# Kernel optimization log

Measured on AMD Instinct MI355X. Metric: run time of the kernel, lower is better.

The kernel has to match this reference:

```python
import jax, jax.numpy as jnp
import numpy as np

B, N, T, D = 4, 1000, 12, 64
HID, EF = 128, 64
E = 64000
STEP = 0.1

def setup_inputs() -> dict:
    key = jax.random.key(0)
    ks = jax.random.split(key, 16)
    s = 0.05
    return {
        'x': jax.random.normal(ks[0], (B, N, T, D), dtype=jnp.float32),
        'batch_idx': jax.random.randint(ks[1], (E,), 0, B, dtype=jnp.int32),
        'sender_idx': jax.random.randint(ks[2], (E,), 0, N, dtype=jnp.int32),
        'receiver_idx': jax.random.randint(ks[3], (E,), 0, N, dtype=jnp.int32),
        'A1_w': jax.random.normal(ks[4], (D, HID), dtype=jnp.float32) * s,
        'A1_b': jax.random.normal(ks[5], (HID,), dtype=jnp.float32) * s,
        'A2_w': jax.random.normal(ks[6], (D, HID), dtype=jnp.float32) * s,
        'A2_b': jax.random.normal(ks[7], (HID,), dtype=jnp.float32) * s,
        'A3_w': jax.random.normal(ks[8], (HID, EF), dtype=jnp.float32) * s,
        'A3_b': jax.random.normal(ks[9], (EF,), dtype=jnp.float32) * s,
        'A4_w': jax.random.normal(ks[10], (EF, D), dtype=jnp.float32) * s,
        'A4_b': jax.random.normal(ks[11], (D,), dtype=jnp.float32) * s,
    }

def reference(x, batch_idx, sender_idx, receiver_idx,
              A1_w, A1_b, A2_w, A2_b, A3_w, A3_b, A4_w, A4_b):
    # x: [B, N, T, D]; edge list gathers (equivalent to adj.nonzero)
    x_sender = x[batch_idx, sender_idx]      # [E, T, D]
    x_receiver = x[batch_idx, receiver_idx]  # [E, T, D]

    def edge_mlp(a, b):
        # A3(relu(A1(a) + A2(b))), applied per edge-time element
        h = jax.nn.relu(a @ A1_w + A1_b + b @ A2_w + A2_b)
        return h @ A3_w + A3_b

    z_ij = edge_mlp(x_sender, x_receiver)
    z_ji = edge_mlp(x_receiver, x_sender)
    v_ij_pre = jax.nn.relu(z_ij - z_ji) @ A4_w + A4_b  # [E, T, D]

    seg_send = batch_idx * N + sender_idx  # [E]
    # numerically-stable segment softmax over outgoing edges of each sender
    max_logits = jax.ops.segment_max(v_ij_pre, seg_send, num_segments=B * N)
    exp_centered = jnp.exp(v_ij_pre - max_logits[seg_send])
    denom = jax.ops.segment_sum(exp_centered, seg_send, num_segments=B * N)
    v_ij = exp_centered / (denom[seg_send] + 1e-12)  # [E, T, D]

    messages = v_ij * x_sender
    seg_recv = batch_idx * N + receiver_idx
    inbound = jax.ops.segment_sum(messages, seg_recv, num_segments=B * N)
    inbound = inbound.reshape(B, N, T, D)

    x_updated = x + STEP * (inbound - x)
    return x_updated, v_ij
```

## Files before the change

kernel.cpp:

```cpp
#include <hip/hip_runtime.h>
#include <math.h>

#define BB 4
#define NN 1000
#define TT 12
#define DD 64
#define HIDN 128
#define EFN 64
#define EE 64000
#define BN (BB*NN)
#define ROWS (BN*TT)
#define TD (TT*DD)
#define STEPF 0.1f
#define MAXSEG 32

typedef __attribute__((ext_vector_type(8))) short bfrag8;
typedef __attribute__((ext_vector_type(8))) unsigned short u16x8;
typedef __attribute__((ext_vector_type(4))) float f32x4;

__device__ __forceinline__ float bf2f(unsigned short u) {
    union { unsigned int i; float f; } p; p.i = ((unsigned int)u) << 16; return p.f;
}
__device__ __forceinline__ unsigned short f2bf(float x) {
    union { float f; unsigned int i; } p; p.f = x;
    unsigned int r = (p.i + 0x7FFFu + ((p.i >> 16) & 1u)) >> 16;
    return (unsigned short)r;
}

__global__ __launch_bounds__(256) void k_zero(int* __restrict__ p, int n) {
    int i = blockIdx.x * 256 + threadIdx.x;
    if (i < n) p[i] = 0;
}

__global__ __launch_bounds__(256) void k_count(const int* __restrict__ bi,
                                               const int* __restrict__ si,
                                               const int* __restrict__ ri,
                                               int* __restrict__ cnt_s,
                                               int* __restrict__ cnt_r) {
    int e = blockIdx.x * 256 + threadIdx.x;
    if (e < EE) {
        int b = bi[e];
        atomicAdd(&cnt_s[b * NN + si[e]], 1);
        atomicAdd(&cnt_r[b * NN + ri[e]], 1);
    }
}

__global__ __launch_bounds__(256) void k_scan(const int* __restrict__ cnt_s,
                                              const int* __restrict__ cnt_r,
                                              int* __restrict__ rp_s, int* __restrict__ rp_r,
                                              int* __restrict__ cur_s, int* __restrict__ cur_r) {
    const int* cnt = blockIdx.x ? cnt_r : cnt_s;
    int* rp  = blockIdx.x ? rp_r  : rp_s;
    int* cur = blockIdx.x ? cur_r : cur_s;
    __shared__ int part[256];
    int tid = threadIdx.x;
    const int chunk = 16;
    int bgn = tid * chunk;
    int end = min(bgn + chunk, BN);
    int s = 0;
    for (int i = bgn; i < end; ++i) s += cnt[i];
    part[tid] = s;
    __syncthreads();
    for (int off = 1; off < 256; off <<= 1) {
        int v = part[tid];
        if (tid >= off) v += part[tid - off];
        __syncthreads();
        part[tid] = v;
        __syncthreads();
    }
    int run = tid ? part[tid - 1] : 0;
    for (int i = bgn; i < end; ++i) { rp[i] = run; cur[i] = run; run += cnt[i]; }
    if (tid == 255) rp[BN] = part[255];
}

__global__ __launch_bounds__(256) void k_fill(const int* __restrict__ bi,
                                              const int* __restrict__ si,
                                              const int* __restrict__ ri,
                                              int* __restrict__ cur_s, int* __restrict__ cur_r,
                                              int* __restrict__ el_s, int* __restrict__ el_r) {
    int e = blockIdx.x * 256 + threadIdx.x;
    if (e < EE) {
        int b = bi[e];
        int ps = atomicAdd(&cur_s[b * NN + si[e]], 1);
        el_s[ps] = e;
        int pr = atomicAdd(&cur_r[b * NN + ri[e]], 1);
        el_r[pr] = e;
    }
}

__global__ __launch_bounds__(256) void k_prep_w(const float* __restrict__ A3_w,
                                                const float* __restrict__ A4_w,
                                                unsigned short* __restrict__ W3f,
                                                unsigned short* __restrict__ W4f) {
    int i = blockIdx.x * 256 + threadIdx.x;
    if (i < 8192) {
        int j = i & 7, lane = (i >> 3) & 63, nt = (i >> 9) & 3, kt = i >> 11;
        int k = kt * 32 + (lane >> 4) * 8 + j;
        int n = nt * 16 + (lane & 15);
        W3f[i] = f2bf(A3_w[k * 64 + n]);
    } else if (i < 12288) {
        int ii = i - 8192;
        int j = ii & 7, lane = (ii >> 3) & 63, nt = (ii >> 9) & 3, kt = ii >> 11;
        int k = kt * 32 + (lane >> 4) * 8 + j;
        int n = nt * 16 + (lane & 15);
        W4f[ii] = f2bf(A4_w[k * 64 + n]);
    }
}

__global__ __launch_bounds__(256) void k_node_proj(const float* __restrict__ x,
                                                   const float* __restrict__ A1_w,
                                                   const float* __restrict__ A1_b,
                                                   const float* __restrict__ A2_w,
                                                   const float* __restrict__ A2_b,
                                                   unsigned short* __restrict__ Q1,
                                                   unsigned short* __restrict__ Q2) {
    __shared__ float xs[16][64];
    int tid = threadIdx.x;
    int row0 = blockIdx.x * 16;
    {
        int i = tid * 4;
        int r = i >> 6, k = i & 63;
        *(float4*)&xs[r][k] = *(const float4*)&x[(size_t)(row0 + r) * 64 + k];
    }
    __syncthreads();
    int h = tid & 127;
    int w = tid >> 7;
    const float* W = w ? A2_w : A1_w;
    float bias = w ? A2_b[h] : A1_b[h];
    float acc[16];
#pragma unroll
    for (int r = 0; r < 16; ++r) acc[r] = 0.f;
    for (int k = 0; k < 64; ++k) {
        float wv = W[k * 128 + h];
#pragma unroll
        for (int r = 0; r < 16; ++r) acc[r] += xs[r][k] * wv;
    }
    unsigned short* Qo = w ? Q2 : Q1;
    for (int r = 0; r < 16; ++r) Qo[(size_t)(row0 + r) * 128 + h] = f2bf(acc[r] + bias);
}

__global__ __launch_bounds__(256) void k_edge_seg(const unsigned short* __restrict__ Q1,
                                                  const unsigned short* __restrict__ Q2,
                                                  const int* __restrict__ bi,
                                                  const int* __restrict__ si,
                                                  const int* __restrict__ ri,
                                                  const int* __restrict__ rp_s,
                                                  const int* __restrict__ el_s,
                                                  const unsigned short* __restrict__ W3f,
                                                  const unsigned short* __restrict__ W4f,
                                                  const float* __restrict__ A4_b,
                                                  float* __restrict__ v) {
    __shared__ unsigned short Vseg[MAXSEG][12][68];
    __shared__ __align__(16) float Hs[4][16][68];

    int seg = blockIdx.x;
    int beg = rp_s[seg], end = rp_s[seg + 1];
    int S = end - beg;
    if (S == 0) return;

    int tid  = threadIdx.x;
    int lane = tid & 63;
    int wv   = tid >> 6;
    int quad = lane >> 4;
    int m    = lane & 15;
    int kbase = quad * 8;

    bfrag8 w3[4][4], w4[2][4];
#pragma unroll
    for (int kt = 0; kt < 4; ++kt)
#pragma unroll
        for (int nt = 0; nt < 4; ++nt)
            w3[kt][nt] = *(const bfrag8*)&W3f[((kt * 4 + nt) * 64 + lane) * 8];
#pragma unroll
    for (int kt = 0; kt < 2; ++kt)
#pragma unroll
        for (int nt = 0; nt < 4; ++nt)
            w4[kt][nt] = *(const bfrag8*)&W4f[((kt * 4 + nt) * 64 + lane) * 8];
    float b4[4];
#pragma unroll
    for (int nt = 0; nt < 4; ++nt) b4[nt] = A4_b[nt * 16 + m];

    const bfrag8 zfrag = {0, 0, 0, 0, 0, 0, 0, 0};

    for (int li = wv; li < S; li += 4) {
        int e = el_s[beg + li];
        int b = bi[e];
        int sn = b * NN + si[e];
        int rn = b * NN + ri[e];

        bfrag8 af[4];
        if (m < 12) {
            const unsigned short* p1s = Q1 + (size_t)sn * (TT * HIDN) + m * 128 + kbase;
            const unsigned short* p2r = Q2 + (size_t)rn * (TT * HIDN) + m * 128 + kbase;
            const unsigned short* p1r = Q1 + (size_t)rn * (TT * HIDN) + m * 128 + kbase;
            const unsigned short* p2s = Q2 + (size_t)sn * (TT * HIDN) + m * 128 + kbase;
#pragma unroll
            for (int kt = 0; kt < 4; ++kt) {
                u16x8 x1 = *(const u16x8*)(p1s + kt * 32);
                u16x8 x2 = *(const u16x8*)(p2r + kt * 32);
                u16x8 x3 = *(const u16x8*)(p1r + kt * 32);
                u16x8 x4 = *(const u16x8*)(p2s + kt * 32);
                union { bfrag8 v; unsigned short u[8]; } fr;
#pragma unroll
                for (int j = 0; j < 8; ++j) {
                    float a = bf2f(x1[j]) + bf2f(x2[j]);
                    float c = bf2f(x3[j]) + bf2f(x4[j]);
                    fr.u[j] = f2bf(fmaxf(a, 0.f) - fmaxf(c, 0.f));
                }
                af[kt] = fr.v;
            }
        } else {
#pragma unroll
            for (int kt = 0; kt < 4; ++kt) af[kt] = zfrag;
        }

        f32x4 acc[4];
#pragma unroll
        for (int nt = 0; nt < 4; ++nt) acc[nt] = (f32x4){0.f, 0.f, 0.f, 0.f};
#pragma unroll
        for (int kt = 0; kt < 4; ++kt)
#pragma unroll
            for (int nt = 0; nt < 4; ++nt)
                acc[nt] = __builtin_amdgcn_mfma_f32_16x16x32_bf16(af[kt], w3[kt][nt], acc[nt], 0, 0, 0);

#pragma unroll
        for (int nt = 0; nt < 4; ++nt)
#pragma unroll
            for (int r = 0; r < 4; ++r)
                Hs[wv][quad * 4 + r][nt * 16 + m] = fmaxf(acc[nt][r], 0.f);

        bfrag8 hf[2];
#pragma unroll
        for (int kt = 0; kt < 2; ++kt) {
            const float* hp = &Hs[wv][m][kt * 32 + kbase];
            float4 h0 = *(const float4*)hp;
            float4 h1 = *(const float4*)(hp + 4);
            union { bfrag8 v; unsigned short u[8]; } fr;
            fr.u[0] = f2bf(h0.x); fr.u[1] = f2bf(h0.y);
            fr.u[2] = f2bf(h0.z); fr.u[3] = f2bf(h0.w);
            fr.u[4] = f2bf(h1.x); fr.u[5] = f2bf(h1.y);
            fr.u[6] = f2bf(h1.z); fr.u[7] = f2bf(h1.w);
            hf[kt] = fr.v;
        }

#pragma unroll
        for (int nt = 0; nt < 4; ++nt) {
            f32x4 o = (f32x4){b4[nt], b4[nt], b4[nt], b4[nt]};
#pragma unroll
            for (int kt = 0; kt < 2; ++kt)
                o = __builtin_amdgcn_mfma_f32_16x16x32_bf16(hf[kt], w4[kt][nt], o, 0, 0, 0);
            if (quad < 3) {
                if (li < MAXSEG) {
#pragma unroll
                    for (int r = 0; r < 4; ++r)
                        Vseg[li][quad * 4 + r][nt * 16 + m] = f2bf(o[r]);
                } else {
                    size_t ebase = (size_t)e * TD;
#pragma unroll
                    for (int r = 0; r < 4; ++r)
                        v[ebase + (quad * 4 + r) * 64 + nt * 16 + m] = o[r];
                }
            }
        }
    }
    __syncthreads();

    int d  = tid & 63;
    int tb = tid >> 6;
    int nL = min(S, MAXSEG);

    float mj[3] = {-1e30f, -1e30f, -1e30f};
    for (int i = 0; i < nL; ++i) {
#pragma unroll
        for (int jj = 0; jj < 3; ++jj)
            mj[jj] = fmaxf(mj[jj], bf2f(Vseg[i][tb + 4 * jj][d]));
    }
    for (int i = MAXSEG; i < S; ++i) {
        size_t ebase = (size_t)el_s[beg + i] * TD;
#pragma unroll
        for (int jj = 0; jj < 3; ++jj)
            mj[jj] = fmaxf(mj[jj], v[ebase + (tb + 4 * jj) * 64 + d]);
    }

    float sj[3] = {0.f, 0.f, 0.f};
    for (int i = 0; i < nL; ++i) {
#pragma unroll
        for (int jj = 0; jj < 3; ++jj)
            sj[jj] += __expf(bf2f(Vseg[i][tb + 4 * jj][d]) - mj[jj]);
    }
    for (int i = MAXSEG; i < S; ++i) {
        size_t ebase = (size_t)el_s[beg + i] * TD;
#pragma unroll
        for (int jj = 0; jj < 3; ++jj)
            sj[jj] += __expf(v[ebase + (tb + 4 * jj) * 64 + d] - mj[jj]);
    }

    float inv[3];
#pragma unroll
    for (int jj = 0; jj < 3; ++jj) inv[jj] = 1.f / (sj[jj] + 1e-12f);

    for (int i = 0; i < nL; ++i) {
        size_t ebase = (size_t)el_s[beg + i] * TD;
#pragma unroll
        for (int jj = 0; jj < 3; ++jj)
            v[ebase + (tb + 4 * jj) * 64 + d] =
                __expf(bf2f(Vseg[i][tb + 4 * jj][d]) - mj[jj]) * inv[jj];
    }
    for (int i = MAXSEG; i < S; ++i) {
        size_t ebase = (size_t)el_s[beg + i] * TD;
#pragma unroll
        for (int jj = 0; jj < 3; ++jj) {
            size_t a = ebase + (tb + 4 * jj) * 64 + d;
            v[a] = __expf(v[a] - mj[jj]) * inv[jj];
        }
    }
}

__global__ __launch_bounds__(256) void k_aggregate(const int* __restrict__ rp_r,
                                                   const int* __restrict__ el_r,
                                                   const int* __restrict__ si,
                                                   const float* __restrict__ x,
                                                   const float* __restrict__ v,
                                                   float* __restrict__ xout) {
    int node = blockIdx.x;
    int beg = rp_r[node], end = rp_r[node + 1];
    int tid = threadIdx.x;
    int b = node / NN;
    __shared__ int e_l[256];
    __shared__ int sb_l[256];
    float acc[3] = {0.f, 0.f, 0.f};
    for (int c = beg; c < end; c += 256) {
        int cnt = min(end - c, 256);
        if (tid < cnt) {
            int e = el_r[c + tid];
            e_l[tid] = e;
            sb_l[tid] = (b * NN + si[e]) * TD;
        }
        __syncthreads();
        for (int i = 0; i < cnt; ++i) {
            size_t vb = (size_t)e_l[i] * TD;
            int sb = sb_l[i];
#pragma unroll
            for (int jj = 0; jj < 3; ++jj) {
                int j = tid + jj * 256;
                acc[jj] += v[vb + j] * x[sb + j];
            }
        }
        __syncthreads();
    }
    size_t nb = (size_t)node * TD;
#pragma unroll
    for (int jj = 0; jj < 3; ++jj) {
        int j = tid + jj * 256;
        float xv = x[nb + j];
        xout[nb + j] = xv + STEPF * (acc[jj] - xv);
    }
}

extern "C" void kernel_launch(void* const* d_in, const int* in_sizes, int n_in,
                              void* d_out, int out_size, void* d_ws, size_t ws_size,
                              hipStream_t stream) {
    const float* x    = (const float*)d_in[0];
    const int*   bi   = (const int*)d_in[1];
    const int*   si   = (const int*)d_in[2];
    const int*   ri   = (const int*)d_in[3];
    const float* A1_w = (const float*)d_in[4];
    const float* A1_b = (const float*)d_in[5];
    const float* A2_w = (const float*)d_in[6];
    const float* A2_b = (const float*)d_in[7];
    const float* A3_w = (const float*)d_in[8];
    const float* A4_w = (const float*)d_in[10];
    const float* A4_b = (const float*)d_in[11];

    float* xout = (float*)d_out;
    float* v    = (float*)d_out + (size_t)BN * TD;

    unsigned short* Q1  = (unsigned short*)d_ws;
    unsigned short* Q2  = Q1 + (size_t)ROWS * HIDN;
    unsigned short* W3f = Q2 + (size_t)ROWS * HIDN;
    unsigned short* W4f = W3f + 8192;
    int* cnt_s = (int*)(W4f + 4096);
    int* cnt_r = cnt_s + BN;
    int* rp_s  = cnt_r + BN;
    int* rp_r  = rp_s + BN + 1;
    int* cur_s = rp_r + BN + 1;
    int* cur_r = cur_s + BN;
    int* el_s  = cur_r + BN;
    int* el_r  = el_s + EE;

    k_zero<<<(2 * BN + 255) / 256, 256, 0, stream>>>(cnt_s, 2 * BN);
    k_count<<<EE / 256, 256, 0, stream>>>(bi, si, ri, cnt_s, cnt_r);
    k_scan<<<2, 256, 0, stream>>>(cnt_s, cnt_r, rp_s, rp_r, cur_s, cur_r);
    k_fill<<<EE / 256, 256, 0, stream>>>(bi, si, ri, cur_s, cur_r, el_s, el_r);
    k_prep_w<<<48, 256, 0, stream>>>(A3_w, A4_w, W3f, W4f);
    k_node_proj<<<ROWS / 16, 256, 0, stream>>>(x, A1_w, A1_b, A2_w, A2_b, Q1, Q2);
    k_edge_seg<<<BN, 256, 0, stream>>>(Q1, Q2, bi, si, ri, rp_s, el_s, W3f, W4f, A4_b, v);
    k_aggregate<<<BN, 256, 0, stream>>>(rp_r, el_r, si, x, v, xout);
}
```

Before: 494.9 us.

## Switch edge MLP to fp16 packed math, hoist sender rows, shrink LDS for occupancy

Intermediates Q1/Q2, weights and the staged logits move from bf16 to fp16, so the pre-activation combine runs as packed half-precision vector adds and max instead of per-element float conversions, and the MFMAs use the f16 variant. The sender row pointers are hoisted out of the edge loop because every edge in a segment shares the same sender and batch, which removes the bi/si gathers. The hidden staging buffer becomes fp16 and MAXSEG drops to 27, shrinking LDS so launch_bounds(256,3) can fit three blocks per CU. The cost is fp16 range and precision on the intermediates, and segments longer than 27 edges spill more often to global memory.

```diff
diff --git a/kernel.cpp b/kernel.cpp
--- a/kernel.cpp
+++ b/kernel.cpp
@@ -12,19 +12,17 @@
 #define ROWS (BN*TT)
 #define TD (TT*DD)
 #define STEPF 0.1f
-#define MAXSEG 32
-
-typedef __attribute__((ext_vector_type(8))) short bfrag8;
-typedef __attribute__((ext_vector_type(8))) unsigned short u16x8;
-typedef __attribute__((ext_vector_type(4))) float f32x4;
-
-__device__ __forceinline__ float bf2f(unsigned short u) {
-    union { unsigned int i; float f; } p; p.i = ((unsigned int)u) << 16; return p.f;
-}
-__device__ __forceinline__ unsigned short f2bf(float x) {
-    union { float f; unsigned int i; } p; p.f = x;
-    unsigned int r = (p.i + 0x7FFFu + ((p.i >> 16) & 1u)) >> 16;
-    return (unsigned short)r;
+#define MAXSEG 27
+
+typedef _Float16 f16x8 __attribute__((ext_vector_type(8)));
+typedef float f32x4 __attribute__((ext_vector_type(4)));
+
+__device__ __forceinline__ unsigned short f2h(float x) {
+    _Float16 h = (_Float16)x;
+    return __builtin_bit_cast(unsigned short, h);
+}
+__device__ __forceinline__ float h2f(unsigned short u) {
+    return (float)__builtin_bit_cast(_Float16, u);
 }
 
 __global__ __launch_bounds__(256) void k_zero(int* __restrict__ p, int n) {
@@ -97,13 +95,13 @@
         int j = i & 7, lane = (i >> 3) & 63, nt = (i >> 9) & 3, kt = i >> 11;
         int k = kt * 32 + (lane >> 4) * 8 + j;
         int n = nt * 16 + (lane & 15);
-        W3f[i] = f2bf(A3_w[k * 64 + n]);
+        W3f[i] = f2h(A3_w[k * 64 + n]);
     } else if (i < 12288) {
         int ii = i - 8192;
         int j = ii & 7, lane = (ii >> 3) & 63, nt = (ii >> 9) & 3, kt = ii >> 11;
         int k = kt * 32 + (lane >> 4) * 8 + j;
         int n = nt * 16 + (lane & 15);
-        W4f[ii] = f2bf(A4_w[k * 64 + n]);
+        W4f[ii] = f2h(A4_w[k * 64 + n]);
     }
 }
 
@@ -136,22 +134,20 @@
         for (int r = 0; r < 16; ++r) acc[r] += xs[r][k] * wv;
     }
     unsigned short* Qo = w ? Q2 : Q1;
-    for (int r = 0; r < 16; ++r) Qo[(size_t)(row0 + r) * 128 + h] = f2bf(acc[r] + bias);
-}
-
-__global__ __launch_bounds__(256) void k_edge_seg(const unsigned short* __restrict__ Q1,
-                                                  const unsigned short* __restrict__ Q2,
-                                                  const int* __restrict__ bi,
-                                                  const int* __restrict__ si,
-                                                  const int* __restrict__ ri,
-                                                  const int* __restrict__ rp_s,
-                                                  const int* __restrict__ el_s,
-                                                  const unsigned short* __restrict__ W3f,
-                                                  const unsigned short* __restrict__ W4f,
-                                                  const float* __restrict__ A4_b,
-                                                  float* __restrict__ v) {
+    for (int r = 0; r < 16; ++r) Qo[(size_t)(row0 + r) * 128 + h] = f2h(acc[r] + bias);
+}
+
+__global__ __launch_bounds__(256, 3) void k_edge_seg(const unsigned short* __restrict__ Q1,
+                                                     const unsigned short* __restrict__ Q2,
+                                                     const int* __restrict__ ri,
+                                                     const int* __restrict__ rp_s,
+                                                     const int* __restrict__ el_s,
+                                                     const unsigned short* __restrict__ W3f,
+                                                     const unsigned short* __restrict__ W4f,
+                                                     const float* __restrict__ A4_b,
+                                                     float* __restrict__ v) {
     __shared__ unsigned short Vseg[MAXSEG][12][68];
-    __shared__ __align__(16) float Hs[4][16][68];
+    __shared__ __align__(16) _Float16 Hs[4][16][72];
 
     int seg = blockIdx.x;
     int beg = rp_s[seg], end = rp_s[seg + 1];
@@ -164,54 +160,54 @@
     int quad = lane >> 4;
     int m    = lane & 15;
     int kbase = quad * 8;
-
-    bfrag8 w3[4][4], w4[2][4];
+    int b    = seg / NN;
+
+    f16x8 w3[4][4], w4[2][4];
 #pragma unroll
     for (int kt = 0; kt < 4; ++kt)
 #pragma unroll
         for (int nt = 0; nt < 4; ++nt)
-            w3[kt][nt] = *(const bfrag8*)&W3f[((kt * 4 + nt) * 64 + lane) * 8];
+            w3[kt][nt] = *(const f16x8*)&W3f[((kt * 4 + nt) * 64 + lane) * 8];
 #pragma unroll
     for (int kt = 0; kt < 2; ++kt)
 #pragma unroll
         for (int nt = 0; nt < 4; ++nt)
-            w4[kt][nt] = *(const bfrag8*)&W4f[((kt * 4 + nt) * 64 + lane) * 8];
+            w4[kt][nt] = *(const f16x8*)&W4f[((kt * 4 + nt) * 64 + lane) * 8];
     float b4[4];
 #pragma unroll
     for (int nt = 0; nt < 4; ++nt) b4[nt] = A4_b[nt * 16 + m];
 
-    const bfrag8 zfrag = {0, 0, 0, 0, 0, 0, 0, 0};
+    const f16x8 hz = {0, 0, 0, 0, 0, 0, 0, 0};
+
+    const unsigned short* ps1 = Q1 + (size_t)seg * (TT * HIDN) + m * 128 + kbase;
+    const unsigned short* ps2 = Q2 + (size_t)seg * (TT * HIDN) + m * 128 + kbase;
 
     for (int li = wv; li < S; li += 4) {
         int e = el_s[beg + li];
-        int b = bi[e];
-        int sn = b * NN + si[e];
         int rn = b * NN + ri[e];
 
-        bfrag8 af[4];
+        f16x8 g[4];
         if (m < 12) {
-            const unsigned short* p1s = Q1 + (size_t)sn * (TT * HIDN) + m * 128 + kbase;
-            const unsigned short* p2r = Q2 + (size_t)rn * (TT * HIDN) + m * 128 + kbase;
-            const unsigned short* p1r = Q1 + (size_t)rn * (TT * HIDN) + m * 128 + kbase;
-            const unsigned short* p2s = Q2 + (size_t)sn * (TT * HIDN) + m * 128 + kbase;
+            const unsigned short* pr1 = Q1 + (size_t)rn * (TT * HIDN) + m * 128 + kbase;
+            const unsigned short* pr2 = Q2 + (size_t)rn * (TT * HIDN) + m * 128 + kbase;
+            f16x8 s1[4], s2[4], r1[4], r2[4];
 #pragma unroll
             for (int kt = 0; kt < 4; ++kt) {
-                u16x8 x1 = *(const u16x8*)(p1s + kt * 32);
-                u16x8 x2 = *(const u16x8*)(p2r + kt * 32);
-                u16x8 x3 = *(const u16x8*)(p1r + kt * 32);
-                u16x8 x4 = *(const u16x8*)(p2s + kt * 32);
-                union { bfrag8 v; unsigned short u[8]; } fr;
-#pragma unroll
-                for (int j = 0; j < 8; ++j) {
-                    float a = bf2f(x1[j]) + bf2f(x2[j]);
-                    float c = bf2f(x3[j]) + bf2f(x4[j]);
-                    fr.u[j] = f2bf(fmaxf(a, 0.f) - fmaxf(c, 0.f));
-                }
-                af[kt] = fr.v;
+                s1[kt] = *(const f16x8*)(ps1 + kt * 32);
+                r2[kt] = *(const f16x8*)(pr2 + kt * 32);
+                r1[kt] = *(const f16x8*)(pr1 + kt * 32);
+                s2[kt] = *(const f16x8*)(ps2 + kt * 32);
+            }
+#pragma unroll
+            for (int kt = 0; kt < 4; ++kt) {
+                f16x8 a = s1[kt] + r2[kt];
+                f16x8 c = r1[kt] + s2[kt];
+                g[kt] = __builtin_elementwise_max(a, hz)
+                      - __builtin_elementwise_max(c, hz);
             }
         } else {
 #pragma unroll
-            for (int kt = 0; kt < 4; ++kt) af[kt] = zfrag;
+            for (int kt = 0; kt < 4; ++kt) g[kt] = hz;
         }
 
         f32x4 acc[4];
@@ -221,39 +217,28 @@
         for (int kt = 0; kt < 4; ++kt)
 #pragma unroll
             for (int nt = 0; nt < 4; ++nt)
-                acc[nt] = __builtin_amdgcn_mfma_f32_16x16x32_bf16(af[kt], w3[kt][nt], acc[nt], 0, 0, 0);
+                acc[nt] = __builtin_amdgcn_mfma_f32_16x16x32_f16(g[kt], w3[kt][nt], acc[nt], 0, 0, 0);
 
 #pragma unroll
         for (int nt = 0; nt < 4; ++nt)
 #pragma unroll
             for (int r = 0; r < 4; ++r)
-                Hs[wv][quad * 4 + r][nt * 16 + m] = fmaxf(acc[nt][r], 0.f);
-
-        bfrag8 hf[2];
-#pragma unroll
-        for (int kt = 0; kt < 2; ++kt) {
-            const float* hp = &Hs[wv][m][kt * 32 + kbase];
-            float4 h0 = *(const float4*)hp;
-            float4 h1 = *(const float4*)(hp + 4);
-            union { bfrag8 v; unsigned short u[8]; } fr;
-            fr.u[0] = f2bf(h0.x); fr.u[1] = f2bf(h0.y);
-            fr.u[2] = f2bf(h0.z); fr.u[3] = f2bf(h0.w);
-            fr.u[4] = f2bf(h1.x); fr.u[5] = f2bf(h1.y);
-            fr.u[6] = f2bf(h1.z); fr.u[7] = f2bf(h1.w);
-            hf[kt] = fr.v;
-        }
+                Hs[wv][quad * 4 + r][nt * 16 + m] = (_Float16)fmaxf(acc[nt][r], 0.f);
+
+        const _Float16* hp = &Hs[wv][m][kbase];
+        f16x8 hf0 = *(const f16x8*)hp;
+        f16x8 hf1 = *(const f16x8*)(hp + 32);
 
 #pragma unroll
         for (int nt = 0; nt < 4; ++nt) {
             f32x4 o = (f32x4){b4[nt], b4[nt], b4[nt], b4[nt]};
-#pragma unroll
-            for (int kt = 0; kt < 2; ++kt)
-                o = __builtin_amdgcn_mfma_f32_16x16x32_bf16(hf[kt], w4[kt][nt], o, 0, 0, 0);
+            o = __builtin_amdgcn_mfma_f32_16x16x32_f16(hf0, w4[0][nt], o, 0, 0, 0);
+            o = __builtin_amdgcn_mfma_f32_16x16x32_f16(hf1, w4[1][nt], o, 0, 0, 0);
             if (quad < 3) {
                 if (li < MAXSEG) {
 #pragma unroll
                     for (int r = 0; r < 4; ++r)
-                        Vseg[li][quad * 4 + r][nt * 16 + m] = f2bf(o[r]);
+                        Vseg[li][quad * 4 + r][nt * 16 + m] = f2h(o[r]);
                 } else {
                     size_t ebase = (size_t)e * TD;
 #pragma unroll
@@ -273,7 +258,7 @@
     for (int i = 0; i < nL; ++i) {
 #pragma unroll
         for (int jj = 0; jj < 3; ++jj)
-            mj[jj] = fmaxf(mj[jj], bf2f(Vseg[i][tb + 4 * jj][d]));
+            mj[jj] = fmaxf(mj[jj], h2f(Vseg[i][tb + 4 * jj][d]));
     }
     for (int i = MAXSEG; i < S; ++i) {
         size_t ebase = (size_t)el_s[beg + i] * TD;
@@ -286,7 +271,7 @@
     for (int i = 0; i < nL; ++i) {
 #pragma unroll
         for (int jj = 0; jj < 3; ++jj)
-            sj[jj] += __expf(bf2f(Vseg[i][tb + 4 * jj][d]) - mj[jj]);
+            sj[jj] += __expf(h2f(Vseg[i][tb + 4 * jj][d]) - mj[jj]);
     }
     for (int i = MAXSEG; i < S; ++i) {
         size_t ebase = (size_t)el_s[beg + i] * TD;
@@ -304,7 +289,7 @@
 #pragma unroll
         for (int jj = 0; jj < 3; ++jj)
             v[ebase + (tb + 4 * jj) * 64 + d] =
-                __expf(bf2f(Vseg[i][tb + 4 * jj][d]) - mj[jj]) * inv[jj];
+                __expf(h2f(Vseg[i][tb + 4 * jj][d]) - mj[jj]) * inv[jj];
     }
     for (int i = MAXSEG; i < S; ++i) {
         size_t ebase = (size_t)el_s[beg + i] * TD;
@@ -394,6 +379,6 @@
     k_fill<<<EE / 256, 256, 0, stream>>>(bi, si, ri, cur_s, cur_r, el_s, el_r);
     k_prep_w<<<48, 256, 0, stream>>>(A3_w, A4_w, W3f, W4f);
     k_node_proj<<<ROWS / 16, 256, 0, stream>>>(x, A1_w, A1_b, A2_w, A2_b, Q1, Q2);
-    k_edge_seg<<<BN, 256, 0, stream>>>(Q1, Q2, bi, si, ri, rp_s, el_s, W3f, W4f, A4_b, v);
+    k_edge_seg<<<BN, 256, 0, stream>>>(Q1, Q2, ri, rp_s, el_s, W3f, W4f, A4_b, v);
     k_aggregate<<<BN, 256, 0, stream>>>(rp_r, el_r, si, x, v, xout);
 }
```

New measurement: 533.5 us. +7.8%, slower.
